# Performance work log

Hardware: AMD Instinct MI355X
Metric: run time of the kernel (lower is better)

The kernel has to match this reference:

```python
import jax, jax.numpy as jnp
import numpy as np

NUM_HEADS = 16
HEAD_DIM = 128  # embed_dim 2048 / 16 heads


def setup_inputs() -> dict:
    key = jax.random.key(0)
    x = jax.random.normal(key, (2, 2048, 2048), dtype=jnp.float32)
    return {"x": x}


def reference(x):
    # EvoAttn forward: V-only causal self-attention (q = k = v = reshaped x).
    B, L, E = x.shape
    H, D = NUM_HEADS, HEAD_DIM
    v = x.reshape(B, L, H, D).transpose(0, 2, 1, 3)  # (B, H, L, D)
    scale = 1.0 / jnp.sqrt(jnp.asarray(D, dtype=x.dtype))
    scores = jnp.einsum("bhqd,bhkd->bhqk", v, v) * scale  # (B, H, L, L)
    causal = jnp.tril(jnp.ones((L, L), dtype=bool))
    scores = jnp.where(causal[None, None], scores, jnp.asarray(-jnp.inf, dtype=scores.dtype))
    p = jax.nn.softmax(scores, axis=-1)
    y = jnp.einsum("bhqk,bhkd->bhqd", p, v)  # (B, H, L, D)
    return y.transpose(0, 2, 1, 3).reshape(B, L, E)
```

## Files before the change

### kernel.cpp

```cpp
#include <hip/hip_runtime.h>
#include <hip/hip_bf16.h>


#define TL 2048
#define TE 2048
#define TD 128
#define KB 64
#define NTILES 32
#define TILE_B 16384
#define KV_REGION (32 * NTILES * TILE_B)
#define WS_NEED (2u * (unsigned)KV_REGION)

typedef __attribute__((ext_vector_type(8))) short bf16x8;
typedef __attribute__((ext_vector_type(4))) float f32x4;
typedef __attribute__((ext_vector_type(8))) unsigned short u16x8;
typedef __attribute__((ext_vector_type(4))) unsigned short u16x4;

#define SCALE_LOG2E 0.12751879f

__device__ __forceinline__ unsigned short f2bf(float f) {
  __hip_bfloat16 h = __float2bfloat16(f);
  return __builtin_bit_cast(unsigned short, h);
}

__device__ __forceinline__ f32x4 mfma16(bf16x8 a, bf16x8 b, f32x4 c) {
  return __builtin_amdgcn_mfma_f32_16x16x32_bf16(a, b, c, 0, 0, 0);
}

__device__ __forceinline__ void gl_lds16(const void* g, void* l) {
  __builtin_amdgcn_global_load_lds(
      (__attribute__((address_space(1))) void*)(g),
      (__attribute__((address_space(3))) void*)(l), 16, 0, 0);
}

__global__ void __launch_bounds__(256)
prepack(const float* __restrict__ x, char* __restrict__ wsb) {
  const int bid = blockIdx.x;
  const int kt = bid & 31;
  const int bh = bid >> 5;
  const int b = bh >> 4;
  const int h = bh & 15;
  const float* src = x + (size_t)b * TL * TE + h * TD + (size_t)kt * KB * TE;
  const int t = threadIdx.x;
  const int kr = (t >> 4) << 2;
  const int d0 = (t & 15) << 3;
  unsigned short c[4][8];
#pragma unroll
  for (int rr = 0; rr < 4; ++rr) {
    const float* p = src + (kr + rr) * TE + d0;
    const float4 a = *(const float4*)p;
    const float4 bb = *(const float4*)(p + 4);
    c[rr][0] = f2bf(a.x);  c[rr][1] = f2bf(a.y);  c[rr][2] = f2bf(a.z);  c[rr][3] = f2bf(a.w);
    c[rr][4] = f2bf(bb.x); c[rr][5] = f2bf(bb.y); c[rr][6] = f2bf(bb.z); c[rr][7] = f2bf(bb.w);
  }
  char* gkv = wsb + (size_t)bid * TILE_B;
  const int kt2 = kr >> 4;
  const int q0r = kr & 15;
  const int cc_ = (t & 15) >> 2;
  const int gg_ = (t & 15) & 3;
#pragma unroll
  for (int rr = 0; rr < 4; ++rr) {
    u16x8 o = {c[rr][0], c[rr][1], c[rr][2], c[rr][3],
               c[rr][4], c[rr][5], c[rr][6], c[rr][7]};
    const int off = (((kt2 * 4 + cc_) * 64 + gg_ * 16 + (q0r + rr)) << 4);
    *(u16x8*)(gkv + off) = o;
  }
  char* gkt = wsb + KV_REGION + (size_t)bid * TILE_B;
  const int half = kr >> 5;
  const int g = (kr >> 3) & 3;
  const int j0 = kr & 7;
#pragma unroll
  for (int cc = 0; cc < 8; ++cc) {
    const int d = d0 + cc;
    u16x4 o = {c[0][cc], c[1][cc], c[2][cc], c[3][cc]};
    const int off = (((half * 8 + (d >> 4)) * 64 + g * 16 + (d & 15)) << 4) + j0 * 2;
    *(u16x4*)(gkt + off) = o;
  }
}

__global__ void __launch_bounds__(256)
evo_attn2(const char* __restrict__ wsb, float* __restrict__ out) {
  __shared__ char smem[3 * TILE_B + 8192];

  const int t = threadIdx.x;
  const int lane = t & 63;
  const int w = t >> 6;
  const int g = lane >> 4;
  const int q15 = lane & 15;

  const int blk = blockIdx.x;
  const int bh = (blk & 7) * 4 + (blk >> 7);
  const int a = (blk >> 3) & 15;
  const int b = bh >> 4;
  const int h = bh & 15;

  const char* gkv = wsb + (size_t)bh * (NTILES * TILE_B);
  const char* gkt = wsb + KV_REGION + (size_t)bh * (NTILES * TILE_B);
  char* plw = smem + 3 * TILE_B + w * 2048;
  const char* kvtb = smem + 2 * TILE_B;
  const int l16 = lane * 16;

#define STAGE_KV(BUFI, KT)                                                 \
  {                                                                        \
    char* dst_ = smem + (BUFI) * TILE_B + (t >> 6) * 1024;                 \
    const char* src_ = gkv + (size_t)(KT) * TILE_B + t * 16;               \
    _Pragma("unroll")                                                      \
    for (int i_ = 0; i_ < 4; ++i_) gl_lds16(src_ + i_ * 4096, dst_ + i_ * 4096); \
  }
#define STAGE_KVT(KT)                                                      \
  {                                                                        \
    char* dst_ = smem + 2 * TILE_B + (t >> 6) * 1024;                      \
    const char* src_ = gkt + (size_t)(KT) * TILE_B + t * 16;               \
    _Pragma("unroll")                                                      \
    for (int i_ = 0; i_ < 4; ++i_) gl_lds16(src_ + i_ * 4096, dst_ + i_ * 4096); \
  }

#pragma unroll 1
  for (int seg = 0; seg < 2; ++seg) {
    const int qt = seg ? (31 - a) : a;
    const int nt = qt + 1;

    STAGE_KV(0, qt);
    if (nt > 1) STAGE_KV(1, 0);
    STAGE_KVT(qt);
    asm volatile("s_waitcnt vmcnt(0)" ::: "memory");
    __builtin_amdgcn_s_barrier();
    asm volatile("" ::: "memory");

    bf16x8 qf[4];
#pragma unroll
    for (int c = 0; c < 4; ++c)
      qf[c] = *(const bf16x8*)(smem + (w * 4 + c) * 1024 + l16);

    f32x4 acc[8];
#pragma unroll
    for (int dt = 0; dt < 8; ++dt) acc[dt] = (f32x4){0.f, 0.f, 0.f, 0.f};
    float mrun = -1e30f;
    float lrun = 0.f;

    for (int s = 0; s < nt; ++s) {
      if (s > 0) {
        asm volatile("s_waitcnt vmcnt(8)" ::: "memory");
        __builtin_amdgcn_s_barrier();
        asm volatile("" ::: "memory");
      }
      const char* kv = smem + (s & 1) * TILE_B;

      float sv[16];
      __builtin_amdgcn_s_setprio(1);
#pragma unroll
      for (int kt2 = 0; kt2 < 4; ++kt2) {
        f32x4 st = (f32x4){0.f, 0.f, 0.f, 0.f};
#pragma unroll
        for (int c = 0; c < 4; ++c) {
          bf16x8 kf = *(const bf16x8*)(kv + (kt2 * 4 + c) * 1024 + l16);
          st = mfma16(kf, qf[c], st);
        }
#pragma unroll
        for (int r = 0; r < 4; ++r) sv[kt2 * 4 + r] = st[r];
      }
      __builtin_amdgcn_s_setprio(0);

      if (s == 0) {
        const int qrel = 16 * w + q15;
#pragma unroll
        for (int kt2 = 0; kt2 < 4; ++kt2)
#pragma unroll
          for (int r = 0; r < 4; ++r)
            if (kt2 * 16 + g * 4 + r > qrel) sv[kt2 * 4 + r] = -1e30f;
      }

      float m0 = fmaxf(fmaxf(sv[0], sv[1]), fmaxf(sv[2], sv[3]));
      float m1 = fmaxf(fmaxf(sv[4], sv[5]), fmaxf(sv[6], sv[7]));
      float m2 = fmaxf(fmaxf(sv[8], sv[9]), fmaxf(sv[10], sv[11]));
      float m3 = fmaxf(fmaxf(sv[12], sv[13]), fmaxf(sv[14], sv[15]));
      float tmax = fmaxf(fmaxf(m0, m1), fmaxf(m2, m3));
      tmax = fmaxf(tmax, __shfl_xor(tmax, 16));
      tmax = fmaxf(tmax, __shfl_xor(tmax, 32));

      float pf[16];
      if (__all(tmax <= mrun)) {
        const float nmc = -mrun * SCALE_LOG2E;
#pragma unroll
        for (int i = 0; i < 16; ++i) pf[i] = exp2f(fmaf(sv[i], SCALE_LOG2E, nmc));
      } else {
        const float mnew = fmaxf(mrun, tmax);
        const float al = exp2f((mrun - mnew) * SCALE_LOG2E);
        mrun = mnew;
        const float nmc = -mnew * SCALE_LOG2E;
#pragma unroll
        for (int i = 0; i < 16; ++i) pf[i] = exp2f(fmaf(sv[i], SCALE_LOG2E, nmc));
        lrun *= al;
        float ar[4];
#pragma unroll
        for (int r = 0; r < 4; ++r) ar[r] = __shfl(al, g * 4 + r);
#pragma unroll
        for (int dt = 0; dt < 8; ++dt)
#pragma unroll
          for (int r = 0; r < 4; ++r) acc[dt][r] *= ar[r];
      }
      {
        float s01 = (pf[0] + pf[1]) + (pf[2] + pf[3]);
        float s23 = (pf[4] + pf[5]) + (pf[6] + pf[7]);
        float s45 = (pf[8] + pf[9]) + (pf[10] + pf[11]);
        float s67 = (pf[12] + pf[13]) + (pf[14] + pf[15]);
        lrun += (s01 + s23) + (s45 + s67);
      }

      {
        const int wb = q15 * 16 + (g & 1) * 8;
#pragma unroll
        for (int kt2 = 0; kt2 < 4; ++kt2) {
          u16x4 o = {f2bf(pf[kt2 * 4]), f2bf(pf[kt2 * 4 + 1]),
                     f2bf(pf[kt2 * 4 + 2]), f2bf(pf[kt2 * 4 + 3])};
          *(u16x4*)(plw + (kt2 * 2 + (g >> 1)) * 256 + wb) = o;
        }
      }
      asm volatile("s_waitcnt lgkmcnt(0)" ::: "memory");

      if (s > 0) {
        if (s + 1 < nt) asm volatile("s_waitcnt vmcnt(4)" ::: "memory");
        else            asm volatile("s_waitcnt vmcnt(0)" ::: "memory");
        __builtin_amdgcn_s_barrier();
        asm volatile("" ::: "memory");
      }

      bf16x8 pa0 = *(const bf16x8*)(plw + g * 256 + q15 * 16);
      bf16x8 pa1 = *(const bf16x8*)(plw + (4 + g) * 256 + q15 * 16);
      __builtin_amdgcn_s_setprio(1);
#pragma unroll
      for (int dt = 0; dt < 8; ++dt) {
        bf16x8 vb0 = *(const bf16x8*)(kvtb + dt * 1024 + l16);
        bf16x8 vb1 = *(const bf16x8*)(kvtb + (8 + dt) * 1024 + l16);
        acc[dt] = mfma16(pa0, vb0, acc[dt]);
        acc[dt] = mfma16(pa1, vb1, acc[dt]);
      }
      __builtin_amdgcn_s_setprio(0);

      __builtin_amdgcn_s_barrier();
      asm volatile("" ::: "memory");
      if (s + 1 < nt) STAGE_KVT(s);
      if (s + 2 < nt) STAGE_KV(s & 1, s + 1);
    }

    lrun += __shfl_xor(lrun, 16);
    lrun += __shfl_xor(lrun, 32);
    const float inv = 1.f / lrun;
    float ir[4];
#pragma unroll
    for (int r = 0; r < 4; ++r) ir[r] = __shfl(inv, g * 4 + r);

    float* ob = out + ((size_t)b * TL + qt * 64 + 16 * w) * TE + h * TD;
#pragma unroll
    for (int dt = 0; dt < 8; ++dt)
#pragma unroll
      for (int r = 0; r < 4; ++r)
        ob[(g * 4 + r) * TE + dt * 16 + q15] = acc[dt][r] * ir[r];

    __builtin_amdgcn_s_barrier();
    asm volatile("" ::: "memory");
  }
}

__device__ __forceinline__ bf16x8 ld256s(const unsigned short* base, int row, int inrow) {
  const int off = (row * 256 + inrow) ^ ((row & 7) << 4);
  return *(const bf16x8*)((const char*)base + off);
}
__device__ __forceinline__ bf16x8 ld128s(const unsigned short* base, int row, int inrow) {
  const int off = (row * 128 + inrow) ^ ((row & 7) << 4);
  return *(const bf16x8*)((const char*)base + off);
}

__device__ __forceinline__ void stage_tile_fb(const float* __restrict__ src,
                                              unsigned short* kv, unsigned short* kvt,
                                              int t) {
  const int kr = (t >> 4) << 2;
  const int d0 = (t & 15) << 3;
  unsigned short c[4][8];
#pragma unroll
  for (int rr = 0; rr < 4; ++rr) {
    const float* p = src + (kr + rr) * TE + d0;
    const float4 a = *(const float4*)p;
    const float4 b = *(const float4*)(p + 4);
    c[rr][0] = f2bf(a.x); c[rr][1] = f2bf(a.y); c[rr][2] = f2bf(a.z); c[rr][3] = f2bf(a.w);
    c[rr][4] = f2bf(b.x); c[rr][5] = f2bf(b.y); c[rr][6] = f2bf(b.z); c[rr][7] = f2bf(b.w);
  }
#pragma unroll
  for (int rr = 0; rr < 4; ++rr) {
    const int r = kr + rr;
    u16x8 o = {c[rr][0], c[rr][1], c[rr][2], c[rr][3],
               c[rr][4], c[rr][5], c[rr][6], c[rr][7]};
    const int off = (r * 256 + d0 * 2) ^ ((r & 7) << 4);
    *(u16x8*)((char*)kv + off) = o;
  }
#pragma unroll
  for (int cc = 0; cc < 8; ++cc) {
    const int d = d0 + cc;
    u16x4 o = {c[0][cc], c[1][cc], c[2][cc], c[3][cc]};
    const int off = (d * 128 + kr * 2) ^ ((d & 7) << 4);
    *(u16x4*)((char*)kvt + off) = o;
  }
}

__global__ void __launch_bounds__(256)
evo_attn(const float* __restrict__ x, float* __restrict__ out) {
  __shared__ unsigned short kv[KB * TD];
  __shared__ unsigned short kvt[TD * KB];
  __shared__ unsigned short pl[4 * 16 * KB];

  const int t = threadIdx.x;
  const int lane = t & 63;
  const int w = t >> 6;
  const int g = lane >> 4;
  const int q15 = lane & 15;

  const int bh = blockIdx.x & 31;
  const int qt = 31 - (blockIdx.x >> 5);
  const int b = bh >> 4;
  const int h = bh & 15;
  const float* xb = x + (size_t)b * TL * TE + h * TD;
  const int q0 = qt * KB;

  stage_tile_fb(xb + (size_t)q0 * TE, kv, kvt, t);
  __syncthreads();

  bf16x8 qf[4];
#pragma unroll
  for (int c = 0; c < 4; ++c)
    qf[c] = ld256s(kv, 16 * w + q15, c * 64 + g * 16);

  f32x4 acc[8];
#pragma unroll
  for (int dt = 0; dt < 8; ++dt) acc[dt] = (f32x4){0.f, 0.f, 0.f, 0.f};
  float mrun = -1e30f;
  float lrun = 0.f;
  unsigned short* plw = pl + w * (16 * KB);

  for (int s = 0; s <= qt; ++s) {
    if (s > 0) {
      __syncthreads();
      stage_tile_fb(xb + (size_t)(s - 1) * KB * TE, kv, kvt, t);
      __syncthreads();
    }
    float sv[16];
#pragma unroll
    for (int kt2 = 0; kt2 < 4; ++kt2) {
      f32x4 st = (f32x4){0.f, 0.f, 0.f, 0.f};
#pragma unroll
      for (int c = 0; c < 4; ++c) {
        bf16x8 kf = ld256s(kv, kt2 * 16 + q15, c * 64 + g * 16);
        st = mfma16(kf, qf[c], st);
      }
#pragma unroll
      for (int r = 0; r < 4; ++r) sv[kt2 * 4 + r] = st[r] * SCALE_LOG2E;
    }
    if (s == 0) {
      const int qrel = 16 * w + q15;
#pragma unroll
      for (int kt2 = 0; kt2 < 4; ++kt2)
#pragma unroll
        for (int r = 0; r < 4; ++r)
          if (kt2 * 16 + g * 4 + r > qrel) sv[kt2 * 4 + r] = -1e30f;
    }
    float tmax = sv[0];
#pragma unroll
    for (int i = 1; i < 16; ++i) tmax = fmaxf(tmax, sv[i]);
    tmax = fmaxf(tmax, __shfl_xor(tmax, 16));
    tmax = fmaxf(tmax, __shfl_xor(tmax, 32));
    const float mnew = fmaxf(mrun, tmax);
    const float al = exp2f(mrun - mnew);
    mrun = mnew;
    float psum = 0.f;
    unsigned short pb[16];
#pragma unroll
    for (int i = 0; i < 16; ++i) {
      const float p = exp2f(sv[i] - mnew);
      psum += p;
      pb[i] = f2bf(p);
    }
    lrun = lrun * al + psum;
#pragma unroll
    for (int kt2 = 0; kt2 < 4; ++kt2) {
      u16x4 o = {pb[kt2 * 4], pb[kt2 * 4 + 1], pb[kt2 * 4 + 2], pb[kt2 * 4 + 3]};
      const int off = (q15 * 128 + kt2 * 32 + g * 8) ^ ((q15 & 7) << 4);
      *(u16x4*)((char*)plw + off) = o;
    }
    asm volatile("s_waitcnt lgkmcnt(0)" ::: "memory");
    float ar[4];
#pragma unroll
    for (int r = 0; r < 4; ++r) ar[r] = __shfl(al, g * 4 + r);
#pragma unroll
    for (int dt = 0; dt < 8; ++dt)
#pragma unroll
      for (int r = 0; r < 4; ++r) acc[dt][r] *= ar[r];
    bf16x8 pa0 = ld128s(plw, q15, g * 16);
    bf16x8 pa1 = ld128s(plw, q15, 64 + g * 16);
#pragma unroll
    for (int dt = 0; dt < 8; ++dt) {
      bf16x8 vb0 = ld128s(kvt, dt * 16 + q15, g * 16);
      bf16x8 vb1 = ld128s(kvt, dt * 16 + q15, 64 + g * 16);
      acc[dt] = mfma16(pa0, vb0, acc[dt]);
      acc[dt] = mfma16(pa1, vb1, acc[dt]);
    }
  }

  lrun += __shfl_xor(lrun, 16);
  lrun += __shfl_xor(lrun, 32);
  const float inv = 1.f / lrun;
  float ir[4];
#pragma unroll
  for (int r = 0; r < 4; ++r) ir[r] = __shfl(inv, g * 4 + r);
  float* ob = out + ((size_t)b * TL + q0 + 16 * w) * TE + h * TD;
#pragma unroll
  for (int dt = 0; dt < 8; ++dt)
#pragma unroll
    for (int r = 0; r < 4; ++r)
      ob[(g * 4 + r) * TE + dt * 16 + q15] = acc[dt][r] * ir[r];
}

extern "C" void kernel_launch(void* const* d_in, const int* in_sizes, int n_in,
                              void* d_out, int out_size, void* d_ws, size_t ws_size,
                              hipStream_t stream) {
  const float* x = (const float*)d_in[0];
  float* out = (float*)d_out;
  (void)in_sizes; (void)n_in; (void)out_size;
  if (ws_size >= (size_t)WS_NEED) {
    char* wsb = (char*)d_ws;
    prepack<<<dim3(1024), dim3(256), 0, stream>>>(x, wsb);
    evo_attn2<<<dim3(512), dim3(256), 0, stream>>>(wsb, out);
  } else {
    evo_attn<<<dim3(1024), dim3(256), 0, stream>>>(x, out);
  }
}
```

Before: 92.71 us.

## Rewrite attention kernel with 32x32 MFMA, split-K waves, and register P

```diff
diff --git a/kernel.cpp b/kernel.cpp
--- a/kernel.cpp
+++ b/kernel.cpp
@@ -13,8 +13,11 @@
 
 typedef __attribute__((ext_vector_type(8))) short bf16x8;
 typedef __attribute__((ext_vector_type(4))) float f32x4;
+typedef __attribute__((ext_vector_type(16))) float f32x16;
 typedef __attribute__((ext_vector_type(8))) unsigned short u16x8;
 typedef __attribute__((ext_vector_type(4))) unsigned short u16x4;
+typedef __attribute__((ext_vector_type(2))) unsigned int u32x2;
+typedef __attribute__((ext_vector_type(4))) unsigned int u32x4;
 
 #define SCALE_LOG2E 0.12751879f
 
@@ -25,12 +28,21 @@
 
 __device__ __forceinline__ f32x4 mfma16(bf16x8 a, bf16x8 b, f32x4 c) {
   return __builtin_amdgcn_mfma_f32_16x16x32_bf16(a, b, c, 0, 0, 0);
+}
+__device__ __forceinline__ f32x16 mfma32(bf16x8 a, bf16x8 b, f32x16 c) {
+  return __builtin_amdgcn_mfma_f32_32x32x16_bf16(a, b, c, 0, 0, 0);
 }
 
 __device__ __forceinline__ void gl_lds16(const void* g, void* l) {
   __builtin_amdgcn_global_load_lds(
       (__attribute__((address_space(1))) void*)(g),
       (__attribute__((address_space(3))) void*)(l), 16, 0, 0);
+}
+
+__device__ __forceinline__ unsigned cvtpk(float lo, float hi) {
+  unsigned r;
+  asm("v_cvt_pk_bf16_f32 %0, %1, %2" : "=v"(r) : "v"(lo), "v"(hi));
+  return r;
 }
 
 __global__ void __launch_bounds__(256)
@@ -54,39 +66,41 @@
     c[rr][4] = f2bf(bb.x); c[rr][5] = f2bf(bb.y); c[rr][6] = f2bf(bb.z); c[rr][7] = f2bf(bb.w);
   }
   char* gkv = wsb + (size_t)bid * TILE_B;
-  const int kt2 = kr >> 4;
-  const int q0r = kr & 15;
-  const int cc_ = (t & 15) >> 2;
-  const int gg_ = (t & 15) & 3;
+  const int dseg = d0 >> 4;
+  const int hi = (d0 >> 3) & 1;
 #pragma unroll
   for (int rr = 0; rr < 4; ++rr) {
+    const int k = kr + rr;
     u16x8 o = {c[rr][0], c[rr][1], c[rr][2], c[rr][3],
                c[rr][4], c[rr][5], c[rr][6], c[rr][7]};
-    const int off = (((kt2 * 4 + cc_) * 64 + gg_ * 16 + (q0r + rr)) << 4);
+    const int off = ((((k >> 5) * 8 + dseg) * 64) + hi * 32 + (k & 31)) << 4;
     *(u16x8*)(gkv + off) = o;
   }
   char* gkt = wsb + KV_REGION + (size_t)bid * TILE_B;
-  const int half = kr >> 5;
-  const int g = (kr >> 3) & 3;
+  const int ks = kr >> 5;
+  const int kc = (kr >> 4) & 1;
+  const int hi2 = (kr >> 3) & 1;
   const int j0 = kr & 7;
 #pragma unroll
   for (int cc = 0; cc < 8; ++cc) {
     const int d = d0 + cc;
     u16x4 o = {c[0][cc], c[1][cc], c[2][cc], c[3][cc]};
-    const int off = (((half * 8 + (d >> 4)) * 64 + g * 16 + (d & 15)) << 4) + j0 * 2;
+    const int off = (((((ks * 2 + kc) * 4 + (d >> 5)) * 64) + hi2 * 32 + (d & 31)) << 4) + j0 * 2;
     *(u16x4*)(gkt + off) = o;
   }
 }
 
 __global__ void __launch_bounds__(256)
-evo_attn2(const char* __restrict__ wsb, float* __restrict__ out) {
-  __shared__ char smem[3 * TILE_B + 8192];
+evo_attn3(const char* __restrict__ wsb, float* __restrict__ out) {
+  __shared__ char smem[4 * TILE_B];
 
   const int t = threadIdx.x;
   const int lane = t & 63;
   const int w = t >> 6;
-  const int g = lane >> 4;
-  const int q15 = lane & 15;
+  const int hi = lane >> 5;
+  const int q31 = lane & 31;
+  const int qhalf = w >> 1;
+  const int ks = w & 1;
 
   const int blk = blockIdx.x;
   const int bh = (blk & 7) * 4 + (blk >> 7);
@@ -96,23 +110,14 @@
 
   const char* gkv = wsb + (size_t)bh * (NTILES * TILE_B);
   const char* gkt = wsb + KV_REGION + (size_t)bh * (NTILES * TILE_B);
-  char* plw = smem + 3 * TILE_B + w * 2048;
-  const char* kvtb = smem + 2 * TILE_B;
   const int l16 = lane * 16;
 
-#define STAGE_KV(BUFI, KT)                                                 \
+#define STG(BASEOFF, REGION, KT)                                           \
   {                                                                        \
-    char* dst_ = smem + (BUFI) * TILE_B + (t >> 6) * 1024;                 \
-    const char* src_ = gkv + (size_t)(KT) * TILE_B + t * 16;               \
+    char* dst_ = smem + (BASEOFF) + w * 4096;                              \
+    const char* src_ = (REGION) + (size_t)(KT) * TILE_B + w * 4096 + l16;  \
     _Pragma("unroll")                                                      \
-    for (int i_ = 0; i_ < 4; ++i_) gl_lds16(src_ + i_ * 4096, dst_ + i_ * 4096); \
-  }
-#define STAGE_KVT(KT)                                                      \
-  {                                                                        \
-    char* dst_ = smem + 2 * TILE_B + (t >> 6) * 1024;                      \
-    const char* src_ = gkt + (size_t)(KT) * TILE_B + t * 16;               \
-    _Pragma("unroll")                                                      \
-    for (int i_ = 0; i_ < 4; ++i_) gl_lds16(src_ + i_ * 4096, dst_ + i_ * 4096); \
+    for (int i_ = 0; i_ < 4; ++i_) gl_lds16(src_ + i_ * 1024, dst_ + i_ * 1024); \
   }
 
 #pragma unroll 1
@@ -120,143 +125,190 @@
     const int qt = seg ? (31 - a) : a;
     const int nt = qt + 1;
 
-    STAGE_KV(0, qt);
-    if (nt > 1) STAGE_KV(1, 0);
-    STAGE_KVT(qt);
-    asm volatile("s_waitcnt vmcnt(0)" ::: "memory");
+    STG(0, gkv, qt);
+    STG(2 * TILE_B, gkt, qt);
+
+    bf16x8 qf[8];
+    f32x16 acc[4];
+#pragma unroll
+    for (int dt = 0; dt < 4; ++dt)
+#pragma unroll
+      for (int r = 0; r < 16; ++r) acc[dt][r] = 0.f;
+    float mrun = -1e30f;
+    float lrun = 0.f;
+
+    for (int s = 0; s < nt; ++s) {
+      asm volatile("s_waitcnt vmcnt(0)" ::: "memory");
+      __builtin_amdgcn_s_barrier();
+      asm volatile("" ::: "memory");
+
+      if (s == 0) {
+#pragma unroll
+        for (int d = 0; d < 8; ++d)
+          qf[d] = *(const bf16x8*)(smem + (qhalf * 8 + d) * 1024 + l16);
+      }
+      if (s + 1 < nt) {
+        STG(((s + 1) & 1) * TILE_B, gkv, s);
+        STG(2 * TILE_B + ((s + 1) & 1) * TILE_B, gkt, s);
+      }
+      const char* kb = smem + (s & 1) * TILE_B;
+      const char* vbb = smem + 2 * TILE_B + (s & 1) * TILE_B;
+      const bool inactive = (s == 0) && (qhalf == 0) && (ks == 1);
+
+      if (!inactive) {
+        f32x16 st;
+#pragma unroll
+        for (int r = 0; r < 16; ++r) st[r] = 0.f;
+        __builtin_amdgcn_s_setprio(1);
+#pragma unroll
+        for (int d = 0; d < 8; ++d) {
+          bf16x8 kf = *(const bf16x8*)(kb + (ks * 8 + d) * 1024 + l16);
+          st = mfma32(kf, qf[d], st);
+        }
+        __builtin_amdgcn_s_setprio(0);
+
+        float sv[16];
+#pragma unroll
+        for (int r = 0; r < 16; ++r) sv[r] = st[r];
+
+        if (s == 0) {
+#pragma unroll
+          for (int r = 0; r < 16; ++r) {
+            const int krow = ks * 32 + (r & 3) + 8 * (r >> 2) + 4 * hi;
+            if (krow > qhalf * 32 + q31) sv[r] = -1e30f;
+          }
+        }
+
+        float m0 = fmaxf(fmaxf(sv[0], sv[1]), fmaxf(sv[2], sv[3]));
+        float m1 = fmaxf(fmaxf(sv[4], sv[5]), fmaxf(sv[6], sv[7]));
+        float m2 = fmaxf(fmaxf(sv[8], sv[9]), fmaxf(sv[10], sv[11]));
+        float m3 = fmaxf(fmaxf(sv[12], sv[13]), fmaxf(sv[14], sv[15]));
+        float tmax = fmaxf(fmaxf(m0, m1), fmaxf(m2, m3));
+        tmax = fmaxf(tmax, __shfl_xor(tmax, 32));
+
+        float pf[16];
+        if (__all(tmax <= mrun)) {
+          const float nmc = -mrun * SCALE_LOG2E;
+#pragma unroll
+          for (int r = 0; r < 16; ++r) pf[r] = exp2f(fmaf(sv[r], SCALE_LOG2E, nmc));
+        } else {
+          const float mnew = fmaxf(mrun, tmax);
+          const float al = exp2f((mrun - mnew) * SCALE_LOG2E);
+          mrun = mnew;
+          const float nmc = -mnew * SCALE_LOG2E;
+#pragma unroll
+          for (int r = 0; r < 16; ++r) pf[r] = exp2f(fmaf(sv[r], SCALE_LOG2E, nmc));
+          lrun *= al;
+          float ar[16];
+#pragma unroll
+          for (int r = 0; r < 16; ++r)
+            ar[r] = __shfl(al, (r & 3) + 8 * (r >> 2) + 4 * hi);
+#pragma unroll
+          for (int dt = 0; dt < 4; ++dt)
+#pragma unroll
+            for (int r = 0; r < 16; ++r) acc[dt][r] *= ar[r];
+        }
+        {
+          float s01 = (pf[0] + pf[1]) + (pf[2] + pf[3]);
+          float s23 = (pf[4] + pf[5]) + (pf[6] + pf[7]);
+          float s45 = (pf[8] + pf[9]) + (pf[10] + pf[11]);
+          float s67 = (pf[12] + pf[13]) + (pf[14] + pf[15]);
+          lrun += (s01 + s23) + (s45 + s67);
+        }
+
+        bf16x8 pa0, pa1;
+        {
+          unsigned A = cvtpk(pf[0], pf[1]), B = cvtpk(pf[2], pf[3]);
+          unsigned C = cvtpk(pf[4], pf[5]), D = cvtpk(pf[6], pf[7]);
+          u32x2 s0 = __builtin_amdgcn_permlane32_swap(A, C, false, false);
+          u32x2 s1 = __builtin_amdgcn_permlane32_swap(B, D, false, false);
+          u32x4 pw = {s0.x, s1.x, s0.y, s1.y};
+          pa0 = __builtin_bit_cast(bf16x8, pw);
+        }
+        {
+          unsigned A = cvtpk(pf[8], pf[9]), B = cvtpk(pf[10], pf[11]);
+          unsigned C = cvtpk(pf[12], pf[13]), D = cvtpk(pf[14], pf[15]);
+          u32x2 s0 = __builtin_amdgcn_permlane32_swap(A, C, false, false);
+          u32x2 s1 = __builtin_amdgcn_permlane32_swap(B, D, false, false);
+          u32x4 pw = {s0.x, s1.x, s0.y, s1.y};
+          pa1 = __builtin_bit_cast(bf16x8, pw);
+        }
+
+        __builtin_amdgcn_s_setprio(1);
+#pragma unroll
+        for (int dt = 0; dt < 4; ++dt) {
+          bf16x8 vb = *(const bf16x8*)(vbb + ((ks * 2 + 0) * 4 + dt) * 1024 + l16);
+          acc[dt] = mfma32(pa0, vb, acc[dt]);
+        }
+#pragma unroll
+        for (int dt = 0; dt < 4; ++dt) {
+          bf16x8 vb = *(const bf16x8*)(vbb + ((ks * 2 + 1) * 4 + dt) * 1024 + l16);
+          acc[dt] = mfma32(pa1, vb, acc[dt]);
+        }
+        __builtin_amdgcn_s_setprio(0);
+      }
+    }
+
+    lrun += __shfl_xor(lrun, 32);
     __builtin_amdgcn_s_barrier();
     asm volatile("" ::: "memory");
 
-    bf16x8 qf[4];
-#pragma unroll
-    for (int c = 0; c < 4; ++c)
-      qf[c] = *(const bf16x8*)(smem + (w * 4 + c) * 1024 + l16);
-
-    f32x4 acc[8];
-#pragma unroll
-    for (int dt = 0; dt < 8; ++dt) acc[dt] = (f32x4){0.f, 0.f, 0.f, 0.f};
-    float mrun = -1e30f;
-    float lrun = 0.f;
-
-    for (int s = 0; s < nt; ++s) {
-      if (s > 0) {
-        asm volatile("s_waitcnt vmcnt(8)" ::: "memory");
-        __builtin_amdgcn_s_barrier();
-        asm volatile("" ::: "memory");
-      }
-      const char* kv = smem + (s & 1) * TILE_B;
-
-      float sv[16];
-      __builtin_amdgcn_s_setprio(1);
-#pragma unroll
-      for (int kt2 = 0; kt2 < 4; ++kt2) {
-        f32x4 st = (f32x4){0.f, 0.f, 0.f, 0.f};
-#pragma unroll
-        for (int c = 0; c < 4; ++c) {
-          bf16x8 kf = *(const bf16x8*)(kv + (kt2 * 4 + c) * 1024 + l16);
-          st = mfma16(kf, qf[c], st);
-        }
-#pragma unroll
-        for (int r = 0; r < 4; ++r) sv[kt2 * 4 + r] = st[r];
-      }
-      __builtin_amdgcn_s_setprio(0);
-
-      if (s == 0) {
-        const int qrel = 16 * w + q15;
-#pragma unroll
-        for (int kt2 = 0; kt2 < 4; ++kt2)
-#pragma unroll
-          for (int r = 0; r < 4; ++r)
-            if (kt2 * 16 + g * 4 + r > qrel) sv[kt2 * 4 + r] = -1e30f;
-      }
-
-      float m0 = fmaxf(fmaxf(sv[0], sv[1]), fmaxf(sv[2], sv[3]));
-      float m1 = fmaxf(fmaxf(sv[4], sv[5]), fmaxf(sv[6], sv[7]));
-      float m2 = fmaxf(fmaxf(sv[8], sv[9]), fmaxf(sv[10], sv[11]));
-      float m3 = fmaxf(fmaxf(sv[12], sv[13]), fmaxf(sv[14], sv[15]));
-      float tmax = fmaxf(fmaxf(m0, m1), fmaxf(m2, m3));
-      tmax = fmaxf(tmax, __shfl_xor(tmax, 16));
-      tmax = fmaxf(tmax, __shfl_xor(tmax, 32));
-
-      float pf[16];
-      if (__all(tmax <= mrun)) {
-        const float nmc = -mrun * SCALE_LOG2E;
-#pragma unroll
-        for (int i = 0; i < 16; ++i) pf[i] = exp2f(fmaf(sv[i], SCALE_LOG2E, nmc));
-      } else {
-        const float mnew = fmaxf(mrun, tmax);
-        const float al = exp2f((mrun - mnew) * SCALE_LOG2E);
-        mrun = mnew;
-        const float nmc = -mnew * SCALE_LOG2E;
-#pragma unroll
-        for (int i = 0; i < 16; ++i) pf[i] = exp2f(fmaf(sv[i], SCALE_LOG2E, nmc));
-        lrun *= al;
-        float ar[4];
-#pragma unroll
-        for (int r = 0; r < 4; ++r) ar[r] = __shfl(al, g * 4 + r);
-#pragma unroll
-        for (int dt = 0; dt < 8; ++dt)
-#pragma unroll
-          for (int r = 0; r < 4; ++r) acc[dt][r] *= ar[r];
-      }
-      {
-        float s01 = (pf[0] + pf[1]) + (pf[2] + pf[3]);
-        float s23 = (pf[4] + pf[5]) + (pf[6] + pf[7]);
-        float s45 = (pf[8] + pf[9]) + (pf[10] + pf[11]);
-        float s67 = (pf[12] + pf[13]) + (pf[14] + pf[15]);
-        lrun += (s01 + s23) + (s45 + s67);
-      }
-
-      {
-        const int wb = q15 * 16 + (g & 1) * 8;
-#pragma unroll
-        for (int kt2 = 0; kt2 < 4; ++kt2) {
-          u16x4 o = {f2bf(pf[kt2 * 4]), f2bf(pf[kt2 * 4 + 1]),
-                     f2bf(pf[kt2 * 4 + 2]), f2bf(pf[kt2 * 4 + 3])};
-          *(u16x4*)(plw + (kt2 * 2 + (g >> 1)) * 256 + wb) = o;
-        }
-      }
-      asm volatile("s_waitcnt lgkmcnt(0)" ::: "memory");
-
-      if (s > 0) {
-        if (s + 1 < nt) asm volatile("s_waitcnt vmcnt(4)" ::: "memory");
-        else            asm volatile("s_waitcnt vmcnt(0)" ::: "memory");
-        __builtin_amdgcn_s_barrier();
-        asm volatile("" ::: "memory");
-      }
-
-      bf16x8 pa0 = *(const bf16x8*)(plw + g * 256 + q15 * 16);
-      bf16x8 pa1 = *(const bf16x8*)(plw + (4 + g) * 256 + q15 * 16);
-      __builtin_amdgcn_s_setprio(1);
-#pragma unroll
-      for (int dt = 0; dt < 8; ++dt) {
-        bf16x8 vb0 = *(const bf16x8*)(kvtb + dt * 1024 + l16);
-        bf16x8 vb1 = *(const bf16x8*)(kvtb + (8 + dt) * 1024 + l16);
-        acc[dt] = mfma16(pa0, vb0, acc[dt]);
-        acc[dt] = mfma16(pa1, vb1, acc[dt]);
-      }
-      __builtin_amdgcn_s_setprio(0);
-
-      __builtin_amdgcn_s_barrier();
-      asm volatile("" ::: "memory");
-      if (s + 1 < nt) STAGE_KVT(s);
-      if (s + 2 < nt) STAGE_KV(s & 1, s + 1);
-    }
-
-    lrun += __shfl_xor(lrun, 16);
-    lrun += __shfl_xor(lrun, 32);
-    const float inv = 1.f / lrun;
-    float ir[4];
-#pragma unroll
-    for (int r = 0; r < 4; ++r) ir[r] = __shfl(inv, g * 4 + r);
-
-    float* ob = out + ((size_t)b * TL + qt * 64 + 16 * w) * TE + h * TD;
-#pragma unroll
-    for (int dt = 0; dt < 8; ++dt)
-#pragma unroll
-      for (int r = 0; r < 4; ++r)
-        ob[(g * 4 + r) * TE + dt * 16 + q15] = acc[dt][r] * ir[r];
-
+    float* mex = (float*)smem;
+    if (hi == 0) {
+      mex[w * 32 + q31] = mrun;
+      mex[128 + w * 32 + q31] = lrun;
+    }
+    asm volatile("s_waitcnt lgkmcnt(0)" ::: "memory");
+    __builtin_amdgcn_s_barrier();
+    asm volatile("" ::: "memory");
+
+    const int pw_ = w ^ 1;
+    const float mp = mex[pw_ * 32 + q31];
+    const float lp = mex[128 + pw_ * 32 + q31];
+    const float M = fmaxf(mrun, mp);
+    const float as_ = exp2f((mrun - M) * SCALE_LOG2E);
+    const float ap_ = exp2f((mp - M) * SCALE_LOG2E);
+    const float L = as_ * lrun + ap_ * lp;
+    const float sc = as_ / L;
+
+    float scr[16];
+#pragma unroll
+    for (int r = 0; r < 16; ++r)
+      scr[r] = __shfl(sc, (r & 3) + 8 * (r >> 2) + 4 * hi);
+#pragma unroll
+    for (int dt = 0; dt < 4; ++dt)
+#pragma unroll
+      for (int r = 0; r < 16; ++r) acc[dt][r] *= scr[r];
+
+    char* xch = smem + 1024 + qhalf * 17408 + lane * 272;
+    if (ks == 1) {
+#pragma unroll
+      for (int dt = 0; dt < 4; ++dt)
+#pragma unroll
+        for (int rq = 0; rq < 4; ++rq) {
+          f32x4 sl = {acc[dt][rq * 4], acc[dt][rq * 4 + 1],
+                      acc[dt][rq * 4 + 2], acc[dt][rq * 4 + 3]};
+          *(f32x4*)(xch + (dt * 4 + rq) * 16) = sl;
+        }
+    }
+    asm volatile("s_waitcnt lgkmcnt(0)" ::: "memory");
+    __builtin_amdgcn_s_barrier();
+    asm volatile("" ::: "memory");
+
+    if (ks == 0) {
+      float* ob = out + ((size_t)b * TL + qt * 64 + qhalf * 32) * TE + h * TD;
+#pragma unroll
+      for (int dt = 0; dt < 4; ++dt)
+#pragma unroll
+        for (int rq = 0; rq < 4; ++rq) {
+          f32x4 p = *(const f32x4*)(xch + (dt * 4 + rq) * 16);
+#pragma unroll
+          for (int rr = 0; rr < 4; ++rr) {
+            const int row = rr + 8 * rq + 4 * hi;
+            ob[row * TE + dt * 32 + q31] = acc[dt][rq * 4 + rr] + p[rr];
+          }
+        }
+    }
     __builtin_amdgcn_s_barrier();
     asm volatile("" ::: "memory");
   }
@@ -427,7 +479,7 @@
   if (ws_size >= (size_t)WS_NEED) {
     char* wsb = (char*)d_ws;
     prepack<<<dim3(1024), dim3(256), 0, stream>>>(x, wsb);
-    evo_attn2<<<dim3(512), dim3(256), 0, stream>>>(wsb, out);
+    evo_attn3<<<dim3(512), dim3(256), 0, stream>>>(wsb, out);
   } else {
     evo_attn<<<dim3(1024), dim3(256), 0, stream>>>(x, out);
   }
```

New measurement: 146.0 us. +57.5%, slower.

## Load transposed V fragments directly into registers and drop the LDS V tile

Applied to the files above, without the earlier changes.

```diff
diff --git a/kernel.cpp b/kernel.cpp
--- a/kernel.cpp
+++ b/kernel.cpp
@@ -79,8 +79,8 @@
 }
 
 __global__ void __launch_bounds__(256)
-evo_attn2(const char* __restrict__ wsb, float* __restrict__ out) {
-  __shared__ char smem[3 * TILE_B + 8192];
+evo_attn4(const char* __restrict__ wsb, float* __restrict__ out) {
+  __shared__ char smem[2 * TILE_B + 8192];
 
   const int t = threadIdx.x;
   const int lane = t & 63;
@@ -96,8 +96,7 @@
 
   const char* gkv = wsb + (size_t)bh * (NTILES * TILE_B);
   const char* gkt = wsb + KV_REGION + (size_t)bh * (NTILES * TILE_B);
-  char* plw = smem + 3 * TILE_B + w * 2048;
-  const char* kvtb = smem + 2 * TILE_B;
+  char* plw = smem + 2 * TILE_B + w * 2048;
   const int l16 = lane * 16;
 
 #define STAGE_KV(BUFI, KT)                                                 \
@@ -107,12 +106,18 @@
     _Pragma("unroll")                                                      \
     for (int i_ = 0; i_ < 4; ++i_) gl_lds16(src_ + i_ * 4096, dst_ + i_ * 4096); \
   }
-#define STAGE_KVT(KT)                                                      \
+
+#define TIDX(S) (((S) == 0) ? qt : ((S)-1))
+
+  bf16x8 vbr[2][8];
+#define VLOAD(S)                                                           \
   {                                                                        \
-    char* dst_ = smem + 2 * TILE_B + (t >> 6) * 1024;                      \
-    const char* src_ = gkt + (size_t)(KT) * TILE_B + t * 16;               \
+    const char* vt_ = gkt + (size_t)TIDX(S) * TILE_B + l16;                \
     _Pragma("unroll")                                                      \
-    for (int i_ = 0; i_ < 4; ++i_) gl_lds16(src_ + i_ * 4096, dst_ + i_ * 4096); \
+    for (int h_ = 0; h_ < 2; ++h_)                                         \
+      _Pragma("unroll")                                                    \
+      for (int d_ = 0; d_ < 8; ++d_)                                       \
+        vbr[h_][d_] = *(const bf16x8*)(vt_ + (h_ * 8 + d_) * 1024);        \
   }
 
 #pragma unroll 1
@@ -122,8 +127,9 @@
 
     STAGE_KV(0, qt);
     if (nt > 1) STAGE_KV(1, 0);
-    STAGE_KVT(qt);
-    asm volatile("s_waitcnt vmcnt(0)" ::: "memory");
+    VLOAD(0);
+    if (nt > 1) asm volatile("s_waitcnt vmcnt(20)" ::: "memory");
+    else        asm volatile("s_waitcnt vmcnt(16)" ::: "memory");
     __builtin_amdgcn_s_barrier();
     asm volatile("" ::: "memory");
 
@@ -140,7 +146,6 @@
 
     for (int s = 0; s < nt; ++s) {
       if (s > 0) {
-        asm volatile("s_waitcnt vmcnt(8)" ::: "memory");
         __builtin_amdgcn_s_barrier();
         asm volatile("" ::: "memory");
       }
@@ -160,6 +165,10 @@
         for (int r = 0; r < 4; ++r) sv[kt2 * 4 + r] = st[r];
       }
       __builtin_amdgcn_s_setprio(0);
+
+      __builtin_amdgcn_s_barrier();
+      asm volatile("" ::: "memory");
+      if (s + 2 < nt) STAGE_KV(s & 1, s + 1);
 
       if (s == 0) {
         const int qrel = 16 * w + q15;
@@ -218,29 +227,20 @@
       }
       asm volatile("s_waitcnt lgkmcnt(0)" ::: "memory");
 
-      if (s > 0) {
-        if (s + 1 < nt) asm volatile("s_waitcnt vmcnt(4)" ::: "memory");
-        else            asm volatile("s_waitcnt vmcnt(0)" ::: "memory");
-        __builtin_amdgcn_s_barrier();
-        asm volatile("" ::: "memory");
-      }
+      if (s + 2 < nt) asm volatile("s_waitcnt vmcnt(4)" ::: "memory");
+      else            asm volatile("s_waitcnt vmcnt(0)" ::: "memory");
 
       bf16x8 pa0 = *(const bf16x8*)(plw + g * 256 + q15 * 16);
       bf16x8 pa1 = *(const bf16x8*)(plw + (4 + g) * 256 + q15 * 16);
       __builtin_amdgcn_s_setprio(1);
 #pragma unroll
       for (int dt = 0; dt < 8; ++dt) {
-        bf16x8 vb0 = *(const bf16x8*)(kvtb + dt * 1024 + l16);
-        bf16x8 vb1 = *(const bf16x8*)(kvtb + (8 + dt) * 1024 + l16);
-        acc[dt] = mfma16(pa0, vb0, acc[dt]);
-        acc[dt] = mfma16(pa1, vb1, acc[dt]);
+        acc[dt] = mfma16(pa0, vbr[0][dt], acc[dt]);
+        acc[dt] = mfma16(pa1, vbr[1][dt], acc[dt]);
       }
       __builtin_amdgcn_s_setprio(0);
 
-      __builtin_amdgcn_s_barrier();
-      asm volatile("" ::: "memory");
-      if (s + 1 < nt) STAGE_KVT(s);
-      if (s + 2 < nt) STAGE_KV(s & 1, s + 1);
+      if (s + 1 < nt) VLOAD(s + 1);
     }
 
     lrun += __shfl_xor(lrun, 16);
@@ -427,7 +427,7 @@
   if (ws_size >= (size_t)WS_NEED) {
     char* wsb = (char*)d_ws;
     prepack<<<dim3(1024), dim3(256), 0, stream>>>(x, wsb);
-    evo_attn2<<<dim3(512), dim3(256), 0, stream>>>(wsb, out);
+    evo_attn4<<<dim3(512), dim3(256), 0, stream>>>(wsb, out);
   } else {
     evo_attn<<<dim3(1024), dim3(256), 0, stream>>>(x, out);
   }
```

Measured after the change: 142.3 us. +53.5%, slower.

## Process adjacent query-tile pair per 512-thread block sharing streamed K/V tiles

Applied to the files above, without the earlier changes.

```diff
diff --git a/kernel.cpp b/kernel.cpp
--- a/kernel.cpp
+++ b/kernel.cpp
@@ -78,21 +78,25 @@
   }
 }
 
-__global__ void __launch_bounds__(256)
-evo_attn2(const char* __restrict__ wsb, float* __restrict__ out) {
-  __shared__ char smem[3 * TILE_B + 8192];
+__global__ void __launch_bounds__(512)
+evo_attn7(const char* __restrict__ wsb, float* __restrict__ out) {
+  __shared__ char smem[4 * TILE_B];
 
   const int t = threadIdx.x;
   const int lane = t & 63;
   const int w = t >> 6;
   const int g = lane >> 4;
   const int q15 = lane & 15;
+  const int kt2q = w & 3;
 
   const int blk = blockIdx.x;
   const int bh = (blk & 7) * 4 + (blk >> 7);
-  const int a = (blk >> 3) & 15;
+  const int ZIG[16] = {15, 0, 13, 2, 11, 4, 9, 6, 8, 7, 10, 5, 12, 3, 14, 1};
+  const int pj = ZIG[(blk >> 3) & 15];
   const int b = bh >> 4;
   const int h = bh & 15;
+  const int nsteps = 2 * pj + 2;
+  const int qtg = 2 * pj + ((w < 4) ? 1 : 0);
 
   const char* gkv = wsb + (size_t)bh * (NTILES * TILE_B);
   const char* gkt = wsb + KV_REGION + (size_t)bh * (NTILES * TILE_B);
@@ -102,51 +106,51 @@
 
 #define STAGE_KV(BUFI, KT)                                                 \
   {                                                                        \
-    char* dst_ = smem + (BUFI) * TILE_B + (t >> 6) * 1024;                 \
-    const char* src_ = gkv + (size_t)(KT) * TILE_B + t * 16;               \
-    _Pragma("unroll")                                                      \
-    for (int i_ = 0; i_ < 4; ++i_) gl_lds16(src_ + i_ * 4096, dst_ + i_ * 4096); \
+    char* dst_ = smem + (BUFI) * TILE_B + w * 2048;                        \
+    const char* src_ = gkv + (size_t)(KT) * TILE_B + w * 2048 + l16;       \
+    gl_lds16(src_, dst_);                                                  \
+    gl_lds16(src_ + 1024, dst_ + 1024);                                    \
   }
 #define STAGE_KVT(KT)                                                      \
   {                                                                        \
-    char* dst_ = smem + 2 * TILE_B + (t >> 6) * 1024;                      \
-    const char* src_ = gkt + (size_t)(KT) * TILE_B + t * 16;               \
-    _Pragma("unroll")                                                      \
-    for (int i_ = 0; i_ < 4; ++i_) gl_lds16(src_ + i_ * 4096, dst_ + i_ * 4096); \
-  }
-
-#pragma unroll 1
-  for (int seg = 0; seg < 2; ++seg) {
-    const int qt = seg ? (31 - a) : a;
-    const int nt = qt + 1;
-
-    STAGE_KV(0, qt);
-    if (nt > 1) STAGE_KV(1, 0);
-    STAGE_KVT(qt);
-    asm volatile("s_waitcnt vmcnt(0)" ::: "memory");
-    __builtin_amdgcn_s_barrier();
-    asm volatile("" ::: "memory");
-
-    bf16x8 qf[4];
+    char* dst_ = smem + 2 * TILE_B + w * 2048;                             \
+    const char* src_ = gkt + (size_t)(KT) * TILE_B + w * 2048 + l16;       \
+    gl_lds16(src_, dst_);                                                  \
+    gl_lds16(src_ + 1024, dst_ + 1024);                                    \
+  }
+
+  STAGE_KV(0, 0);
+  STAGE_KV(1, 1);
+  STAGE_KVT(0);
+  bf16x8 qf[4];
+  {
+    const char* qsrc = gkv + (size_t)qtg * TILE_B;
 #pragma unroll
     for (int c = 0; c < 4; ++c)
-      qf[c] = *(const bf16x8*)(smem + (w * 4 + c) * 1024 + l16);
-
-    f32x4 acc[8];
-#pragma unroll
-    for (int dt = 0; dt < 8; ++dt) acc[dt] = (f32x4){0.f, 0.f, 0.f, 0.f};
-    float mrun = -1e30f;
-    float lrun = 0.f;
-
-    for (int s = 0; s < nt; ++s) {
-      if (s > 0) {
-        asm volatile("s_waitcnt vmcnt(8)" ::: "memory");
-        __builtin_amdgcn_s_barrier();
-        asm volatile("" ::: "memory");
-      }
-      const char* kv = smem + (s & 1) * TILE_B;
-
-      float sv[16];
+      qf[c] = *(const bf16x8*)(qsrc + (kt2q * 4 + c) * 1024 + l16);
+  }
+  asm volatile("s_waitcnt vmcnt(0)" ::: "memory");
+  __builtin_amdgcn_s_barrier();
+  asm volatile("" ::: "memory");
+
+  f32x4 acc[8];
+#pragma unroll
+  for (int dt = 0; dt < 8; ++dt) acc[dt] = (f32x4){0.f, 0.f, 0.f, 0.f};
+  float mrun = -1e30f;
+  float lrun = 0.f;
+
+  for (int s = 0; s < nsteps; ++s) {
+    if (s > 0) {
+      if (s + 1 < nsteps) asm volatile("s_waitcnt vmcnt(4)" ::: "memory");
+      else                asm volatile("s_waitcnt vmcnt(2)" ::: "memory");
+      __builtin_amdgcn_s_barrier();
+      asm volatile("" ::: "memory");
+    }
+    const char* kv = smem + (s & 1) * TILE_B;
+    const bool active = (s <= qtg);
+
+    float pf[16];
+    if (active) {
       __builtin_amdgcn_s_setprio(1);
 #pragma unroll
       for (int kt2 = 0; kt2 < 4; ++kt2) {
@@ -157,39 +161,38 @@
           st = mfma16(kf, qf[c], st);
         }
 #pragma unroll
-        for (int r = 0; r < 4; ++r) sv[kt2 * 4 + r] = st[r];
+        for (int r = 0; r < 4; ++r) pf[kt2 * 4 + r] = st[r];
       }
       __builtin_amdgcn_s_setprio(0);
 
-      if (s == 0) {
-        const int qrel = 16 * w + q15;
+      if (s == qtg) {
+        const int qrel = 16 * kt2q + q15;
 #pragma unroll
         for (int kt2 = 0; kt2 < 4; ++kt2)
 #pragma unroll
           for (int r = 0; r < 4; ++r)
-            if (kt2 * 16 + g * 4 + r > qrel) sv[kt2 * 4 + r] = -1e30f;
-      }
-
-      float m0 = fmaxf(fmaxf(sv[0], sv[1]), fmaxf(sv[2], sv[3]));
-      float m1 = fmaxf(fmaxf(sv[4], sv[5]), fmaxf(sv[6], sv[7]));
-      float m2 = fmaxf(fmaxf(sv[8], sv[9]), fmaxf(sv[10], sv[11]));
-      float m3 = fmaxf(fmaxf(sv[12], sv[13]), fmaxf(sv[14], sv[15]));
+            if (kt2 * 16 + g * 4 + r > qrel) pf[kt2 * 4 + r] = -1e30f;
+      }
+
+      float m0 = fmaxf(fmaxf(pf[0], pf[1]), fmaxf(pf[2], pf[3]));
+      float m1 = fmaxf(fmaxf(pf[4], pf[5]), fmaxf(pf[6], pf[7]));
+      float m2 = fmaxf(fmaxf(pf[8], pf[9]), fmaxf(pf[10], pf[11]));
+      float m3 = fmaxf(fmaxf(pf[12], pf[13]), fmaxf(pf[14], pf[15]));
       float tmax = fmaxf(fmaxf(m0, m1), fmaxf(m2, m3));
       tmax = fmaxf(tmax, __shfl_xor(tmax, 16));
       tmax = fmaxf(tmax, __shfl_xor(tmax, 32));
 
-      float pf[16];
       if (__all(tmax <= mrun)) {
         const float nmc = -mrun * SCALE_LOG2E;
 #pragma unroll
-        for (int i = 0; i < 16; ++i) pf[i] = exp2f(fmaf(sv[i], SCALE_LOG2E, nmc));
+        for (int i = 0; i < 16; ++i) pf[i] = exp2f(fmaf(pf[i], SCALE_LOG2E, nmc));
       } else {
         const float mnew = fmaxf(mrun, tmax);
         const float al = exp2f((mrun - mnew) * SCALE_LOG2E);
         mrun = mnew;
         const float nmc = -mnew * SCALE_LOG2E;
 #pragma unroll
-        for (int i = 0; i < 16; ++i) pf[i] = exp2f(fmaf(sv[i], SCALE_LOG2E, nmc));
+        for (int i = 0; i < 16; ++i) pf[i] = exp2f(fmaf(pf[i], SCALE_LOG2E, nmc));
         lrun *= al;
         float ar[4];
 #pragma unroll
@@ -217,14 +220,16 @@
         }
       }
       asm volatile("s_waitcnt lgkmcnt(0)" ::: "memory");
-
-      if (s > 0) {
-        if (s + 1 < nt) asm volatile("s_waitcnt vmcnt(4)" ::: "memory");
-        else            asm volatile("s_waitcnt vmcnt(0)" ::: "memory");
-        __builtin_amdgcn_s_barrier();
-        asm volatile("" ::: "memory");
-      }
-
+    }
+
+    if (s > 0) {
+      if (s + 1 < nsteps) asm volatile("s_waitcnt vmcnt(2)" ::: "memory");
+      else                asm volatile("s_waitcnt vmcnt(0)" ::: "memory");
+      __builtin_amdgcn_s_barrier();
+      asm volatile("" ::: "memory");
+    }
+
+    if (active) {
       bf16x8 pa0 = *(const bf16x8*)(plw + g * 256 + q15 * 16);
       bf16x8 pa1 = *(const bf16x8*)(plw + (4 + g) * 256 + q15 * 16);
       __builtin_amdgcn_s_setprio(1);
@@ -236,29 +241,27 @@
         acc[dt] = mfma16(pa1, vb1, acc[dt]);
       }
       __builtin_amdgcn_s_setprio(0);
-
-      __builtin_amdgcn_s_barrier();
-      asm volatile("" ::: "memory");
-      if (s + 1 < nt) STAGE_KVT(s);
-      if (s + 2 < nt) STAGE_KV(s & 1, s + 1);
-    }
-
-    lrun += __shfl_xor(lrun, 16);
-    lrun += __shfl_xor(lrun, 32);
-    const float inv = 1.f / lrun;
-    float ir[4];
-#pragma unroll
-    for (int r = 0; r < 4; ++r) ir[r] = __shfl(inv, g * 4 + r);
-
-    float* ob = out + ((size_t)b * TL + qt * 64 + 16 * w) * TE + h * TD;
-#pragma unroll
-    for (int dt = 0; dt < 8; ++dt)
-#pragma unroll
-      for (int r = 0; r < 4; ++r)
-        ob[(g * 4 + r) * TE + dt * 16 + q15] = acc[dt][r] * ir[r];
+    }
+
+    if (s == qtg) {
+      lrun += __shfl_xor(lrun, 16);
+      lrun += __shfl_xor(lrun, 32);
+      const float inv = 1.f / lrun;
+      float ir[4];
+#pragma unroll
+      for (int r = 0; r < 4; ++r) ir[r] = __shfl(inv, g * 4 + r);
+      float* ob = out + ((size_t)b * TL + qtg * 64 + 16 * kt2q) * TE + h * TD;
+#pragma unroll
+      for (int dt = 0; dt < 8; ++dt)
+#pragma unroll
+        for (int r = 0; r < 4; ++r)
+          ob[(g * 4 + r) * TE + dt * 16 + q15] = acc[dt][r] * ir[r];
+    }
 
     __builtin_amdgcn_s_barrier();
     asm volatile("" ::: "memory");
+    if (s + 1 < nsteps) STAGE_KVT(s + 1);
+    if (s + 2 < nsteps) STAGE_KV(s & 1, s + 2);
   }
 }
 
@@ -427,7 +430,7 @@
   if (ws_size >= (size_t)WS_NEED) {
     char* wsb = (char*)d_ws;
     prepack<<<dim3(1024), dim3(256), 0, stream>>>(x, wsb);
-    evo_attn2<<<dim3(512), dim3(256), 0, stream>>>(wsb, out);
+    evo_attn7<<<dim3(512), dim3(512), 0, stream>>>(wsb, out);
   } else {
     evo_attn<<<dim3(1024), dim3(256), 0, stream>>>(x, out);
   }
```

New measurement: 154.4 us. +66.5%, slower.
